# Kernel tuning notes

Measured on AMD Instinct MI355X. Metric: run time of the kernel, lower is better.

The kernel has to match this reference:

```python
import jax, jax.numpy as jnp
import numpy as np

B, NQ, NP = 4, 8192, 2048
DIM_INP, DIM, HID, OUT, NBLK = 256, 200, 128, 3, 5
VAR = 0.2 ** 2


def setup_inputs() -> dict:
    key = jax.random.key(0)
    ks = jax.random.split(key, 12)
    s = 0.05  # weight scale to keep activations sane
    return {
        "xyz_q": jax.random.uniform(ks[0], (B, NQ, 3), jnp.float32),
        "anchors": jax.random.uniform(ks[1], (B, NP, 3), jnp.float32),
        "anchor_feats": jax.random.normal(ks[2], (B, NP, DIM_INP), jnp.float32),
        "fc0_w": jax.random.normal(ks[3], (DIM_INP, DIM), jnp.float32) * s,
        "fc0_b": jnp.zeros((DIM,), jnp.float32),
        "fc1_w": jax.random.normal(ks[4], (DIM, HID), jnp.float32) * s,
        "fc1_b": jnp.zeros((HID,), jnp.float32),
        "blk_w0": jax.random.normal(ks[5], (NBLK, HID, HID), jnp.float32) * s,
        "blk_b0": jnp.zeros((NBLK, HID), jnp.float32),
        "blk_w1": jax.random.normal(ks[6], (NBLK, HID, HID), jnp.float32) * s,
        "blk_b1": jnp.zeros((NBLK, HID), jnp.float32),
        "fcc_w": jax.random.normal(ks[7], (NBLK, DIM, HID), jnp.float32) * s,
        "fcc_b": jnp.zeros((NBLK, HID), jnp.float32),
        "out_w": jax.random.normal(ks[8], (HID, OUT), jnp.float32) * s,
        "out_b": jnp.zeros((OUT,), jnp.float32),
    }


def reference(xyz_q, anchors, anchor_feats, fc0_w, fc0_b, fc1_w, fc1_b,
              blk_w0, blk_b0, blk_w1, blk_b1, fcc_w, fcc_b, out_w, out_b):
    relu = jax.nn.relu
    # Gaussian-kernel interpolation of anchor features at query points.
    # diff: [B, nq, np, 3]
    diff = anchors[:, None, :, :] - xyz_q[:, :, None, :]
    d = jnp.linalg.norm(diff, axis=-1)                    # [B, nq, np]
    logits = -((d + 1e-5) ** 2) / VAR
    weight = jax.nn.softmax(logits, axis=2)               # exp / sum, stable
    c = jnp.einsum('bqp,bpd->bqd', weight, anchor_feats)  # [B, nq, dim_inp]
    lat = c @ fc0_w + fc0_b                               # [B, nq, dim]
    net = relu(lat) @ fc1_w + fc1_b                       # [B, nq, hid]
    for i in range(NBLK):
        net = net + lat @ fcc_w[i] + fcc_b[i]
        # ResnetBlockFC: x + fc_1(relu(fc_0(relu(x))))
        dx = relu(relu(net) @ blk_w0[i] + blk_b0[i]) @ blk_w1[i] + blk_b1[i]
        net = net + dx
    return relu(net) @ out_w + out_b                      # [B, nq, 3]
```

## Files before the change

### kernel.cpp

```cpp
#include <hip/hip_runtime.h>
#include <math.h>

#define NP     2048
#define NQTOT  8192
#define DIN    256
#define DIM    200
#define HID    128
#define NOUT3  3
#define NBLK   5
#define TQ     32
#define NTHR   256
#define INVVAR 25.0f
#define NKT    (NP / 32)
#define NDT    (DIN / 16)
#define WSCALE 32768.0f
#define NFRAG  760

using f16x8 = __attribute__((ext_vector_type(8))) _Float16;
using f32x4 = __attribute__((ext_vector_type(4))) float;

__device__ __forceinline__ unsigned int pkrtz_u32(float a, float b) {
  auto p = __builtin_amdgcn_cvt_pkrtz(a, b);
  return __builtin_bit_cast(unsigned int, p);
}
__device__ __forceinline__ void pack_f16_2(const float* f, f16x8& h, f16x8& l) {
#pragma unroll
  for (int j = 0; j < 8; ++j) {
    const float v = f[j];
    const _Float16 hh = (_Float16)v;
    h[j] = hh; l[j] = (_Float16)(v - (float)hh);
  }
}
__device__ __forceinline__ void pack_w16(const float* f, f16x8& h, f16x8& l) {
#pragma unroll
  for (int j = 0; j < 8; ++j) {
    const float v = f[j] * WSCALE;
    const _Float16 hh = (_Float16)v;
    h[j] = hh; l[j] = (_Float16)(v - (float)hh);
  }
}
__device__ __forceinline__ void pack_a(const float* f, f16x8& h, f16x8& l) {
  union { f16x8 v; unsigned int u[4]; } H, L;
#pragma unroll
  for (int jp = 0; jp < 4; ++jp) {
    const float a = f[2 * jp], b = f[2 * jp + 1];
    auto hp = __builtin_amdgcn_cvt_pkrtz(a, b);
    H.u[jp] = __builtin_bit_cast(unsigned int, hp);
    L.u[jp] = pkrtz_u32(a - (float)hp[0], b - (float)hp[1]);
  }
  h = H.v; l = L.v;
}
__device__ __forceinline__ unsigned int split_pack(float x) {
  auto hp = __builtin_amdgcn_cvt_pkrtz(x, x);
  return pkrtz_u32(x, x - (float)hp[0]);
}

__device__ __forceinline__ int qsw(int r, int q) {
  return r * TQ + (q ^ (((r >> 2) & 7) << 2));
}
template<int KPAD>
__device__ __forceinline__ int sidx(int q, int k) {
  return q * KPAD + (((k >> 2) ^ (q & 7)) << 2) + (k & 3);
}

template<int KPAD, bool RELU>
__device__ __forceinline__ void store_split4(unsigned int* dst, int k, int qbase, f32x4 v) {
#pragma unroll
  for (int r = 0; r < 4; ++r) {
    float x = v[r];
    if (RELU) x = fmaxf(x, 0.f);
    dst[sidx<KPAD>(qbase + r, k)] = split_pack(x);
  }
}

__global__ __launch_bounds__(NTHR) void pid_packf(const float* __restrict__ F,
                                                  f16x8* __restrict__ wsHi,
                                                  f16x8* __restrict__ wsLo) {
  const int wid = threadIdx.x >> 6, l = threadIdx.x & 63;
  const int tile = blockIdx.x * 4 + wid;
  const int b  = tile >> 10;
  const int kt = (tile >> 4) & 63;
  const int dt = tile & 15;
  const int grp = l >> 4, qn = l & 15;
  const float* src = F + ((size_t)b * NP + kt * 32 + grp * 8) * DIN + dt * 16 + qn;
  float v[8];
#pragma unroll
  for (int j = 0; j < 8; ++j) v[j] = src[(size_t)j * DIN];
  f16x8 h, lo;
  pack_f16_2(v, h, lo);
  const size_t fi = (size_t)tile * 64 + l;
  wsHi[fi] = h; wsLo[fi] = lo;
}

__global__ __launch_bounds__(NTHR) void pid_packw(
    const float* __restrict__ fc0_w, const float* __restrict__ fc1_w,
    const float* __restrict__ fcc_w, const float* __restrict__ blk_w0,
    const float* __restrict__ blk_w1,
    f16x8* __restrict__ Wh, f16x8* __restrict__ Wm) {
  const int wid = threadIdx.x >> 6, l = threadIdx.x & 63;
  const int f = blockIdx.x * 4 + wid;
  if (f >= NFRAG) return;
  const float* src; int Kl, Nl, ks, nt;
  if (f < 104)      { int r = f;       src = fc0_w; Kl = 256; Nl = 200; ks = r / 13; nt = r % 13; }
  else if (f < 160) { int r = f - 104; src = fc1_w; Kl = 200; Nl = 128; ks = r / 8;  nt = r % 8; }
  else if (f < 440) { int r = f - 160; int i = r / 56; r %= 56;
                      src = fcc_w + (size_t)i * DIM * HID; Kl = 200; Nl = 128; ks = r / 8; nt = r % 8; }
  else if (f < 600) { int r = f - 440; int i = r / 32; r %= 32;
                      src = blk_w0 + (size_t)i * HID * HID; Kl = 128; Nl = 128; ks = r / 8; nt = r % 8; }
  else              { int r = f - 600; int i = r / 32; r %= 32;
                      src = blk_w1 + (size_t)i * HID * HID; Kl = 128; Nl = 128; ks = r / 8; nt = r % 8; }
  const int grp = l >> 4, n = nt * 16 + (l & 15);
  f16x8 h, m;
#pragma unroll
  for (int j = 0; j < 8; ++j) {
    const int k = ks * 32 + grp * 8 + j;
    const float v = (k < Kl && n < Nl) ? src[(size_t)k * Nl + n] : 0.f;
    const _Float16 hh = (_Float16)v;
    h[j] = hh; m[j] = (_Float16)(v - (float)hh);
  }
  const size_t fi = (size_t)f * 64 + l;
  Wh[fi] = h; Wm[fi] = m;
}

template<int KS, int NT, int MAXNT, int KPADIN, bool RELUA>
__device__ __forceinline__ void mm_stage(
    const unsigned int* __restrict__ Xs,
    const f16x8* __restrict__ Wh, const f16x8* __restrict__ Wm, int fbase,
    f32x4 acc[2][MAXNT], int wid, int l) {
  const int grp = l >> 4, qn = l & 15;
  f16x8 bhA[MAXNT], bmA[MAXNT], bhB[MAXNT], bmB[MAXNT];

#define LOADF(BH, BM, KSV)                                                    \
  _Pragma("unroll") for (int i = 0; i < MAXNT; ++i) {                         \
    const int nt = wid + i * 4;                                               \
    if (nt < NT) {                                                            \
      const size_t fi = (size_t)(fbase + (KSV) * NT + nt) * 64 + l;           \
      BH[i] = Wh[fi]; BM[i] = Wm[fi];                                         \
    }                                                                         \
  }

#define COMPUTE(KSV, BH, BM)                                                  \
  {                                                                           \
    const int u0 = (KSV) * 8 + grp * 2;                                       \
    f16x8 ah[2], al[2];                                                       \
    _Pragma("unroll") for (int qt = 0; qt < 2; ++qt) {                        \
      const int q = qt * 16 + qn;                                             \
      const unsigned int* row = Xs + q * KPADIN;                              \
      const uint4 lo = *(const uint4*)(row + (((u0) ^ (q & 7)) << 2));        \
      const uint4 hi = *(const uint4*)(row + (((u0 + 1) ^ (q & 7)) << 2));    \
      unsigned int p[8] = {lo.x, lo.y, lo.z, lo.w, hi.x, hi.y, hi.z, hi.w};   \
      if (RELUA) {                                                            \
        _Pragma("unroll") for (int j = 0; j < 8; ++j)                         \
          p[j] = (p[j] & 0x8000u) ? 0u : p[j];                                \
      }                                                                       \
      union { f16x8 v; unsigned int u[4]; } H, L;                             \
      _Pragma("unroll") for (int jp = 0; jp < 4; ++jp) {                      \
        H.u[jp] = __builtin_amdgcn_perm(p[2 * jp + 1], p[2 * jp], 0x05040100u);\
        L.u[jp] = __builtin_amdgcn_perm(p[2 * jp + 1], p[2 * jp], 0x07060302u);\
      }                                                                       \
      ah[qt] = H.v; al[qt] = L.v;                                             \
    }                                                                         \
    _Pragma("unroll") for (int qt = 0; qt < 2; ++qt)                          \
    _Pragma("unroll") for (int i = 0; i < MAXNT; ++i)                         \
      if (wid + i * 4 < NT) {                                                 \
        acc[qt][i] = __builtin_amdgcn_mfma_f32_16x16x32_f16(ah[qt], BH[i], acc[qt][i], 0, 0, 0); \
        acc[qt][i] = __builtin_amdgcn_mfma_f32_16x16x32_f16(ah[qt], BM[i], acc[qt][i], 0, 0, 0); \
        acc[qt][i] = __builtin_amdgcn_mfma_f32_16x16x32_f16(al[qt], BH[i], acc[qt][i], 0, 0, 0); \
      }                                                                       \
  }

  LOADF(bhA, bmA, 0)
#pragma unroll 1
  for (int ks = 0; ks + 1 < KS; ks += 2) {
    LOADF(bhB, bmB, ks + 1)
    COMPUTE(ks, bhA, bmA)
    if (ks + 2 < KS) { LOADF(bhA, bmA, ks + 2) }
    COMPUTE(ks + 1, bhB, bmB)
  }
  if (KS & 1) { COMPUTE(KS - 1, bhA, bmA) }
#undef LOADF
#undef COMPUTE
}

struct SMemV2 {
  union {
    struct { float ax[NP * 3]; float qx[TQ], qy[TQ], qz[TQ]; } a;
    unsigned int lats[32 * 224];
  } r1;
  union {
    unsigned int cTs[32 * 256];
    struct { unsigned int nets[32 * 128]; unsigned int tmps[32 * 128]; } nt;
    float netf[128 * 32];
  } r2;
  float sS[64];
};

__global__ __launch_bounds__(NTHR, 2) void pid_fused_mfma(
    const float* __restrict__ xyz_q, const float* __restrict__ anchors,
    const f16x8* __restrict__ wsFh, const f16x8* __restrict__ wsFl,
    const f16x8* __restrict__ Wh, const f16x8* __restrict__ Wm,
    const float* __restrict__ fc0_b, const float* __restrict__ fc1_b,
    const float* __restrict__ blk_b0, const float* __restrict__ blk_b1,
    const float* __restrict__ fcc_b,
    const float* __restrict__ out_w, const float* __restrict__ out_b,
    float* __restrict__ out) {
  __shared__ SMemV2 sm;
  const int t = threadIdx.x;
  const int bi = blockIdx.x;
  const int batch = bi & 3;
  const int q0 = (bi >> 2) * TQ;

  {
    const float4* src = (const float4*)(anchors + (size_t)batch * NP * 3);
    float4* dst = (float4*)sm.r1.a.ax;
#pragma unroll
    for (int j = 0; j < (NP * 3 / 4) / NTHR; ++j)
      dst[j * NTHR + t] = src[j * NTHR + t];
  }
  if (t < TQ) {
    const float* qp = xyz_q + ((size_t)batch * NQTOT + q0 + t) * 3;
    sm.r1.a.qx[t] = qp[0]; sm.r1.a.qy[t] = qp[1]; sm.r1.a.qz[t] = qp[2];
  }
  __syncthreads();

  const int wid = t >> 6, l = t & 63;
  const int kp = wid & 1;
  const int dh = wid >> 1;
  const int grp = l >> 4, qn = l & 15;
  const float q0x = sm.r1.a.qx[qn],      q0y = sm.r1.a.qy[qn],      q0z = sm.r1.a.qz[qn];
  const float q1x = sm.r1.a.qx[16 + qn], q1y = sm.r1.a.qy[16 + qn], q1z = sm.r1.a.qz[16 + qn];
  const float nC1 = -36.067376f;
  const float nC2 = -7.2134752e-4f;

  const size_t fb = (size_t)batch * (NKT * NDT * 64) + kp * 1024 + dh * 512 + l;
  const f16x8* pH0 = wsFh + fb;  const f16x8* pL0 = wsFl + fb;
  const f16x8* pH1 = pH0 + 256;  const f16x8* pL1 = pL0 + 256;

  f32x4 acc[2][8];
#pragma unroll
  for (int a = 0; a < 2; ++a)
#pragma unroll
    for (int j = 0; j < 8; ++j) acc[a][j] = (f32x4){0.f, 0.f, 0.f, 0.f};
  float s0 = 0.f, s1 = 0.f;

#pragma unroll 1
  for (int kt = kp; kt < NKT; kt += 2) {
    f16x8 bh0[4], bl0[4], bh1[4], bl1[4];
#pragma unroll
    for (int k = 0; k < 4; ++k) { bh0[k] = pH0[k * 64]; bl0[k] = pL0[k * 64]; }
#pragma unroll
    for (int k = 0; k < 4; ++k) { bh1[k] = pH1[k * 64]; bl1[k] = pL1[k * 64]; }

    const int pb = kt * 32 + grp * 8;
    float4 av[6];
    {
      const float4* ap = (const float4*)&sm.r1.a.ax[pb * 3];
#pragma unroll
      for (int j = 0; j < 6; ++j) av[j] = ap[j];
    }
    const float* af = (const float*)av;
    float w8[8];
#pragma unroll
    for (int j = 0; j < 8; ++j) {
      const float dx = af[3 * j] - q0x, dy = af[3 * j + 1] - q0y, dz = af[3 * j + 2] - q0z;
      const float D = fmaf(dx, dx, fmaf(dy, dy, dz * dz));
      const float s = __builtin_amdgcn_sqrtf(D);
      const float u = __builtin_amdgcn_exp2f(fmaf(nC2, s, fmaf(nC1, D, 15.0f)));
      w8[j] = u; s0 += u;
    }
    f16x8 ah0, al0;
    pack_a(w8, ah0, al0);
#pragma unroll
    for (int j = 0; j < 8; ++j) {
      const float dx = af[3 * j] - q1x, dy = af[3 * j + 1] - q1y, dz = af[3 * j + 2] - q1z;
      const float D = fmaf(dx, dx, fmaf(dy, dy, dz * dz));
      const float s = __builtin_amdgcn_sqrtf(D);
      const float u = __builtin_amdgcn_exp2f(fmaf(nC2, s, fmaf(nC1, D, 15.0f)));
      w8[j] = u; s1 += u;
    }
    f16x8 ah1, al1;
    pack_a(w8, ah1, al1);

#define MM3(ACC, AH, AL, BH, BL)                                              \
    ACC = __builtin_amdgcn_mfma_f32_16x16x32_f16(AH, BH, ACC, 0, 0, 0);       \
    ACC = __builtin_amdgcn_mfma_f32_16x16x32_f16(AH, BL, ACC, 0, 0, 0);       \
    ACC = __builtin_amdgcn_mfma_f32_16x16x32_f16(AL, BH, ACC, 0, 0, 0);
#pragma unroll
    for (int k = 0; k < 4; ++k) {
      MM3(acc[0][k], ah0, al0, bh0[k], bl0[k])
      MM3(acc[1][k], ah1, al1, bh0[k], bl0[k])
    }
#pragma unroll
    for (int k = 0; k < 4; ++k) {
      MM3(acc[0][4 + k], ah0, al0, bh1[k], bl1[k])
      MM3(acc[1][4 + k], ah1, al1, bh1[k], bl1[k])
    }
#undef MM3
    pH0 += 2048; pL0 += 2048; pH1 += 2048; pL1 += 2048;
  }

  s0 += __shfl_xor(s0, 16); s0 += __shfl_xor(s0, 32);
  s1 += __shfl_xor(s1, 16); s1 += __shfl_xor(s1, 32);
  if (dh == 0 && l < 16) {
    sm.sS[kp * 32 + qn] = s0;
    sm.sS[kp * 32 + 16 + qn] = s1;
  }
  float4* P = (float4*)sm.r2.cTs;
  if (kp == 0) {
#pragma unroll
    for (int qt2 = 0; qt2 < 2; ++qt2)
#pragma unroll
      for (int d2 = 0; d2 < 8; ++d2)
        P[(qt2 * 16 + dh * 8 + d2) * 64 + grp * 16 + qn] =
            make_float4(acc[qt2][d2][0], acc[qt2][d2][1],
                        acc[qt2][d2][2], acc[qt2][d2][3]);
  }
  __syncthreads();
  if (kp == 1) {
#pragma unroll
    for (int qt2 = 0; qt2 < 2; ++qt2)
#pragma unroll
      for (int d2 = 0; d2 < 8; ++d2) {
        const float4 pv = P[(qt2 * 16 + dh * 8 + d2) * 64 + grp * 16 + qn];
        acc[qt2][d2][0] += pv.x; acc[qt2][d2][1] += pv.y;
        acc[qt2][d2][2] += pv.z; acc[qt2][d2][3] += pv.w;
      }
  } else {
    const int lid = (wid >> 1) * 64 + l;
#pragma unroll
    for (int z = 0; z < 6; ++z) {
      const int idx = lid * 6 + z;
      const int q = idx / 24, kk = 200 + idx % 24;
      sm.r1.lats[sidx<224>(q, kk)] = 0u;
    }
  }
  __syncthreads();
  if (kp == 1) {
    float sc0[4], sc1[4];
#pragma unroll
    for (int r = 0; r < 4; ++r) {
      const int j = grp * 4 + r;
      sc0[r] = __builtin_amdgcn_rcpf(sm.sS[j] + sm.sS[32 + j]);
      sc1[r] = __builtin_amdgcn_rcpf(sm.sS[16 + j] + sm.sS[48 + j]);
    }
#pragma unroll
    for (int d2 = 0; d2 < 8; ++d2) {
      const int k = (dh * 8 + d2) * 16 + qn;
      const f32x4 v0 = {acc[0][d2][0] * sc0[0], acc[0][d2][1] * sc0[1],
                        acc[0][d2][2] * sc0[2], acc[0][d2][3] * sc0[3]};
      store_split4<256, false>(sm.r2.cTs, k, grp * 4, v0);
      const f32x4 v1 = {acc[1][d2][0] * sc1[0], acc[1][d2][1] * sc1[1],
                        acc[1][d2][2] * sc1[2], acc[1][d2][3] * sc1[3]};
      store_split4<256, false>(sm.r2.cTs, k, 16 + grp * 4, v1);
    }
  }
  __syncthreads();

  {
    f32x4 a0[2][4];
#pragma unroll
    for (int i = 0; i < 4; ++i) {
      const int nt = wid + i * 4;
      if (nt < 13) {
        const int n = nt * 16 + qn;
        const float b = (n < 200) ? fc0_b[n] : 0.f;
#pragma unroll
        for (int q2 = 0; q2 < 2; ++q2) a0[q2][i] = (f32x4){b, b, b, b};
      }
    }
    mm_stage<8, 13, 4, 256, false>(sm.r2.cTs, Wh, Wm, 0, a0, wid, l);
#pragma unroll
    for (int q2 = 0; q2 < 2; ++q2)
#pragma unroll
      for (int i = 0; i < 4; ++i) {
        const int nt = wid + i * 4;
        if (nt < 13)
          store_split4<224, false>(sm.r1.lats, nt * 16 + qn, q2 * 16 + grp * 4, a0[q2][i]);
      }
  }
  __syncthreads();

  f32x4 net[2][2];
#pragma unroll
  for (int i = 0; i < 2; ++i) {
    const float b = fc1_b[(wid + i * 4) * 16 + qn];
#pragma unroll
    for (int q2 = 0; q2 < 2; ++q2) net[q2][i] = (f32x4){b, b, b, b};
  }
  mm_stage<7, 8, 2, 224, true>(sm.r1.lats, Wh, Wm, 104, net, wid, l);

#pragma unroll 1
  for (int ib = 0; ib < NBLK; ++ib) {
#pragma unroll
    for (int i = 0; i < 2; ++i) {
      const float b = fcc_b[ib * HID + (wid + i * 4) * 16 + qn];
#pragma unroll
      for (int q2 = 0; q2 < 2; ++q2) net[q2][i] += (f32x4){b, b, b, b};
    }
    mm_stage<7, 8, 2, 224, false>(sm.r1.lats, Wh, Wm, 160 + 56 * ib, net, wid, l);
#pragma unroll
    for (int q2 = 0; q2 < 2; ++q2)
#pragma unroll
      for (int i = 0; i < 2; ++i)
        store_split4<128, true>(sm.r2.nt.nets, (wid + i * 4) * 16 + qn,
                                q2 * 16 + grp * 4, net[q2][i]);
    __syncthreads();
    f32x4 a2[2][2];
#pragma unroll
    for (int i = 0; i < 2; ++i) {
      const float b = blk_b0[ib * HID + (wid + i * 4) * 16 + qn];
#pragma unroll
      for (int q2 = 0; q2 < 2; ++q2) a2[q2][i] = (f32x4){b, b, b, b};
    }
    mm_stage<4, 8, 2, 128, false>(sm.r2.nt.nets, Wh, Wm, 440 + 32 * ib, a2, wid, l);
#pragma unroll
    for (int q2 = 0; q2 < 2; ++q2)
#pragma unroll
      for (int i = 0; i < 2; ++i)
        store_split4<128, true>(sm.r2.nt.tmps, (wid + i * 4) * 16 + qn,
                                q2 * 16 + grp * 4, a2[q2][i]);
    __syncthreads();
#pragma unroll
    for (int i = 0; i < 2; ++i) {
      const float b = blk_b1[ib * HID + (wid + i * 4) * 16 + qn];
#pragma unroll
      for (int q2 = 0; q2 < 2; ++q2) net[q2][i] += (f32x4){b, b, b, b};
    }
    mm_stage<4, 8, 2, 128, false>(sm.r2.nt.tmps, Wh, Wm, 600 + 32 * ib, net, wid, l);
  }
  __syncthreads();

#pragma unroll
  for (int q2 = 0; q2 < 2; ++q2)
#pragma unroll
    for (int i = 0; i < 2; ++i) {
      const int n = (wid + i * 4) * 16 + qn;
      *(float4*)&sm.r2.netf[n * 32 + q2 * 16 + grp * 4] =
          make_float4(net[q2][i][0], net[q2][i][1], net[q2][i][2], net[q2][i][3]);
    }
  __syncthreads();
  if (t < TQ * NOUT3) {
    const int q = t / NOUT3, n = t - q * NOUT3;
    float s = out_b[n];
#pragma unroll 8
    for (int k = 0; k < HID; ++k)
      s = fmaf(fmaxf(sm.r2.netf[k * 32 + q], 0.f), out_w[k * NOUT3 + n], s);
    out[((size_t)batch * NQTOT + q0 + q) * NOUT3 + n] = s;
  }
}

template<int K, bool RELUX, bool ACCY>
__device__ __forceinline__ void stage_h128(const float* __restrict__ X,
                                           const float* __restrict__ Wg,
                                           const float* __restrict__ bg,
                                           float* __restrict__ Y, int t) {
  const int qg = t & 7, ng = t >> 3;
  const int n0 = ng * 4, q0 = qg * 4;
  const float4 bv = *(const float4*)&bg[n0];
  const float br[4] = {bv.x, bv.y, bv.z, bv.w};
  float acc[4][4];
#pragma unroll
  for (int j = 0; j < 4; ++j) {
    if (ACCY) {
      const float4 yv = *(const float4*)&Y[qsw(n0 + j, q0)];
      acc[0][j] = yv.x + br[j]; acc[1][j] = yv.y + br[j];
      acc[2][j] = yv.z + br[j]; acc[3][j] = yv.w + br[j];
    } else {
      acc[0][j] = br[j]; acc[1][j] = br[j]; acc[2][j] = br[j]; acc[3][j] = br[j];
    }
  }
#pragma unroll 2
  for (int k0 = 0; k0 < K; k0 += 8) {
    float4 wr[8];
#pragma unroll
    for (int kk = 0; kk < 8; ++kk)
      wr[kk] = *(const float4*)&Wg[(size_t)(k0 + kk) * HID + n0];
#pragma unroll
    for (int kk = 0; kk < 8; ++kk) {
      float4 xv = *(const float4*)&X[qsw(k0 + kk, q0)];
      if (RELUX) {
        xv.x = fmaxf(xv.x, 0.f); xv.y = fmaxf(xv.y, 0.f);
        xv.z = fmaxf(xv.z, 0.f); xv.w = fmaxf(xv.w, 0.f);
      }
      const float xr[4] = {xv.x, xv.y, xv.z, xv.w};
      const float wl[4] = {wr[kk].x, wr[kk].y, wr[kk].z, wr[kk].w};
#pragma unroll
      for (int i = 0; i < 4; ++i)
#pragma unroll
        for (int j = 0; j < 4; ++j)
          acc[i][j] = fmaf(xr[i], wl[j], acc[i][j]);
    }
  }
#pragma unroll
  for (int j = 0; j < 4; ++j)
    *(float4*)&Y[qsw(n0 + j, q0)] =
        make_float4(acc[0][j], acc[1][j], acc[2][j], acc[3][j]);
}

__device__ __forceinline__ void stage_fc0v(const float* __restrict__ X,
                                           const float* __restrict__ Wg,
                                           const float* __restrict__ bg,
                                           float* __restrict__ Y, int t) {
  const int qg = t & 7, ng = t >> 3;
  const int n0 = ng * 8, q0 = qg * 4;
  const bool act = (ng < 25);
  float acc[4][8];
  if (act) {
    const float4 b0 = *(const float4*)&bg[n0];
    const float4 b1 = *(const float4*)&bg[n0 + 4];
    const float br[8] = {b0.x, b0.y, b0.z, b0.w, b1.x, b1.y, b1.z, b1.w};
#pragma unroll
    for (int j = 0; j < 8; ++j)
#pragma unroll
      for (int i = 0; i < 4; ++i) acc[i][j] = br[j];
  }
#pragma unroll 2
  for (int k0 = 0; k0 < DIN; k0 += 4) {
    if (act) {
      float4 wa[4], wb[4];
#pragma unroll
      for (int kk = 0; kk < 4; ++kk) {
        wa[kk] = *(const float4*)&Wg[(size_t)(k0 + kk) * DIM + n0];
        wb[kk] = *(const float4*)&Wg[(size_t)(k0 + kk) * DIM + n0 + 4];
      }
#pragma unroll
      for (int kk = 0; kk < 4; ++kk) {
        const float4 xv = *(const float4*)&X[qsw(k0 + kk, q0)];
        const float xr[4] = {xv.x, xv.y, xv.z, xv.w};
        const float wl[8] = {wa[kk].x, wa[kk].y, wa[kk].z, wa[kk].w,
                             wb[kk].x, wb[kk].y, wb[kk].z, wb[kk].w};
#pragma unroll
        for (int i = 0; i < 4; ++i)
#pragma unroll
          for (int j = 0; j < 8; ++j)
            acc[i][j] = fmaf(xr[i], wl[j], acc[i][j]);
      }
    }
  }
  if (act) {
#pragma unroll
    for (int j = 0; j < 8; ++j)
      *(float4*)&Y[qsw(n0 + j, q0)] =
          make_float4(acc[0][j], acc[1][j], acc[2][j], acc[3][j]);
  }
}

struct SA1 {
  float ax[NP * 3];
  float qx[TQ], qy[TQ], qz[TQ], m[TQ];
  float sred[8 * TQ];
};
struct SB1 {
  float lat[DIM * TQ];
  union {
    float cT[DIN * TQ];
    struct { float net[HID * TQ]; float tmp[HID * TQ]; } nt;
  } u;
};
struct SMem1 { union { SA1 a; SB1 b; } s; float sS[TQ]; };

__global__ __launch_bounds__(NTHR, 2) void pid_fused_vec(
    const float* __restrict__ xyz_q, const float* __restrict__ anchors,
    const f16x8* __restrict__ wsFh, const f16x8* __restrict__ wsFl,
    const float* __restrict__ fc0_w, const float* __restrict__ fc0_b,
    const float* __restrict__ fc1_w, const float* __restrict__ fc1_b,
    const float* __restrict__ blk_w0, const float* __restrict__ blk_b0,
    const float* __restrict__ blk_w1, const float* __restrict__ blk_b1,
    const float* __restrict__ fcc_w, const float* __restrict__ fcc_b,
    const float* __restrict__ out_w, const float* __restrict__ out_b,
    float* __restrict__ out) {
  __shared__ SMem1 sm;
  const int t = threadIdx.x;
  const int bi = blockIdx.x;
  const int batch = bi & 3;
  const int q0 = (bi >> 2) * TQ;

  {
    const float4* src = (const float4*)(anchors + (size_t)batch * NP * 3);
    float4* dst = (float4*)sm.s.a.ax;
#pragma unroll
    for (int j = 0; j < (NP * 3 / 4) / NTHR; ++j)
      dst[j * NTHR + t] = src[j * NTHR + t];
  }
  if (t < TQ) {
    const float* qp = xyz_q + ((size_t)batch * NQTOT + q0 + t) * 3;
    sm.s.a.qx[t] = qp[0]; sm.s.a.qy[t] = qp[1]; sm.s.a.qz[t] = qp[2];
  }
  __syncthreads();
  {
    const int q = t & 31, g = t >> 5;
    const float qxv = sm.s.a.qx[q], qyv = sm.s.a.qy[q], qzv = sm.s.a.qz[q];
    float mloc = 3.0e38f;
    const float* az = sm.s.a.ax + g * 256 * 3;
    for (int pi = 0; pi < 256; ++pi) {
      const float dx = az[pi * 3 + 0] - qxv;
      const float dy = az[pi * 3 + 1] - qyv;
      const float dz = az[pi * 3 + 2] - qzv;
      mloc = fminf(mloc, fmaf(dx, dx, fmaf(dy, dy, dz * dz)));
    }
    sm.s.a.sred[g * TQ + q] = mloc;
  }
  __syncthreads();
  if (t < TQ) {
    float mv = sm.s.a.sred[t];
#pragma unroll
    for (int g = 1; g < 8; ++g) mv = fminf(mv, sm.s.a.sred[g * TQ + t]);
    const float dmin = sqrtf(mv) + 1e-5f;
    sm.s.a.m[t] = -dmin * dmin * INVVAR;
  }
  __syncthreads();

  const int wid = t >> 6, l = t & 63;
  const int qt = wid & 1;
  const int dgb = (wid >> 1) * 8;
  const int grp = l >> 4, qn = l & 15;
  const float qxv = sm.s.a.qx[qt * 16 + qn];
  const float qyv = sm.s.a.qy[qt * 16 + qn];
  const float qzv = sm.s.a.qz[qt * 16 + qn];
  const float negm = -sm.s.a.m[qt * 16 + qn];
  const f16x8* BH = wsFh + (size_t)batch * NKT * NDT * 64;
  const f16x8* BL = wsFl + (size_t)batch * NKT * NDT * 64;

  f32x4 acc[8];
#pragma unroll
  for (int j = 0; j < 8; ++j) acc[j] = (f32x4){0.f, 0.f, 0.f, 0.f};
  float ssum = 0.f;
#pragma unroll 1
  for (int kt = 0; kt < NKT; ++kt) {
    f16x8 bh[8], bl[8];
#pragma unroll
    for (int d2 = 0; d2 < 8; ++d2) {
      const size_t fi = ((size_t)kt * NDT + dgb + d2) * 64 + l;
      bh[d2] = BH[fi]; bl[d2] = BL[fi];
    }
    const int pb = kt * 32 + grp * 8;
    float4 av[6];
    {
      const float4* ap = (const float4*)&sm.s.a.ax[pb * 3];
#pragma unroll
      for (int j = 0; j < 6; ++j) av[j] = ap[j];
    }
    const float* af = (const float*)av;
    float w8[8];
#pragma unroll
    for (int j = 0; j < 8; ++j) {
      const float dx = af[3 * j] - qxv, dy = af[3 * j + 1] - qyv, dz = af[3 * j + 2] - qzv;
      const float d = sqrtf(fmaf(dx, dx, fmaf(dy, dy, dz * dz))) + 1e-5f;
      const float u = __expf(fmaf(d * d, -INVVAR, negm));
      w8[j] = u; ssum += u;
    }
    f16x8 ah, al;
    pack_w16(w8, ah, al);
#pragma unroll
    for (int d2 = 0; d2 < 8; ++d2)
      acc[d2] = __builtin_amdgcn_mfma_f32_16x16x32_f16(ah, bh[d2], acc[d2], 0, 0, 0);
#pragma unroll
    for (int d2 = 0; d2 < 8; ++d2)
      acc[d2] = __builtin_amdgcn_mfma_f32_16x16x32_f16(ah, bl[d2], acc[d2], 0, 0, 0);
#pragma unroll
    for (int d2 = 0; d2 < 8; ++d2)
      acc[d2] = __builtin_amdgcn_mfma_f32_16x16x32_f16(al, bh[d2], acc[d2], 0, 0, 0);
  }
  ssum += __shfl_xor(ssum, 16);
  ssum += __shfl_xor(ssum, 32);
  if (wid < 2 && grp == 0) sm.sS[qt * 16 + qn] = ssum;
  __syncthreads();
  float sc[4];
#pragma unroll
  for (int r = 0; r < 4; ++r)
    sc[r] = (1.0f / WSCALE) / sm.sS[qt * 16 + grp * 4 + r];
#pragma unroll
  for (int d2 = 0; d2 < 8; ++d2) {
    const int d = (dgb + d2) * 16 + qn;
    *(float4*)&sm.s.b.u.cT[qsw(d, qt * 16 + grp * 4)] =
        make_float4(acc[d2][0] * sc[0], acc[d2][1] * sc[1],
                    acc[d2][2] * sc[2], acc[d2][3] * sc[3]);
  }
  __syncthreads();

  stage_fc0v(sm.s.b.u.cT, fc0_w, fc0_b, sm.s.b.lat, t);
  __syncthreads();
  stage_h128<DIM, true, false>(sm.s.b.lat, fc1_w, fc1_b, sm.s.b.u.nt.net, t);
  __syncthreads();
#pragma unroll 1
  for (int i = 0; i < NBLK; ++i) {
    stage_h128<DIM, false, true>(sm.s.b.lat, fcc_w + (size_t)i * DIM * HID,
                                 fcc_b + i * HID, sm.s.b.u.nt.net, t);
    __syncthreads();
    stage_h128<HID, true, false>(sm.s.b.u.nt.net, blk_w0 + (size_t)i * HID * HID,
                                 blk_b0 + i * HID, sm.s.b.u.nt.tmp, t);
    __syncthreads();
    stage_h128<HID, true, true>(sm.s.b.u.nt.tmp, blk_w1 + (size_t)i * HID * HID,
                                blk_b1 + i * HID, sm.s.b.u.nt.net, t);
    __syncthreads();
  }
  if (t < TQ * NOUT3) {
    const int q = t / NOUT3, n = t - q * NOUT3;
    float s = out_b[n];
    const float* net = sm.s.b.u.nt.net;
#pragma unroll 8
    for (int k = 0; k < HID; ++k)
      s = fmaf(fmaxf(net[k * TQ + (q ^ (((k >> 2) & 7) << 2))], 0.f),
               out_w[k * NOUT3 + n], s);
    out[((size_t)batch * NQTOT + q0 + q) * NOUT3 + n] = s;
  }
}

extern "C" void kernel_launch(void* const* d_in, const int* in_sizes, int n_in,
                              void* d_out, int out_size, void* d_ws, size_t ws_size,
                              hipStream_t stream) {
  (void)in_sizes; (void)n_in; (void)out_size;
  const float* xyz_q        = (const float*)d_in[0];
  const float* anchors      = (const float*)d_in[1];
  const float* anchor_feats = (const float*)d_in[2];
  const float* fc0_w        = (const float*)d_in[3];
  const float* fc0_b        = (const float*)d_in[4];
  const float* fc1_w        = (const float*)d_in[5];
  const float* fc1_b        = (const float*)d_in[6];
  const float* blk_w0       = (const float*)d_in[7];
  const float* blk_b0       = (const float*)d_in[8];
  const float* blk_w1       = (const float*)d_in[9];
  const float* blk_b1       = (const float*)d_in[10];
  const float* fcc_w        = (const float*)d_in[11];
  const float* fcc_b        = (const float*)d_in[12];
  const float* out_w        = (const float*)d_in[13];
  const float* out_b        = (const float*)d_in[14];
  float* out = (float*)d_out;

  const size_t F_BYTES = (size_t)4 * NKT * NDT * 64 * 16;
  const size_t W_BYTES = (size_t)NFRAG * 64 * 16;
  f16x8* wsFh = (f16x8*)d_ws;
  f16x8* wsFl = (f16x8*)((char*)d_ws + F_BYTES);
  f16x8* Wh   = (f16x8*)((char*)d_ws + 2 * F_BYTES);
  f16x8* Wm   = (f16x8*)((char*)d_ws + 2 * F_BYTES + W_BYTES);

  hipLaunchKernelGGL(pid_packf, dim3(1024), dim3(NTHR), 0, stream,
                     anchor_feats, wsFh, wsFl);
  if (ws_size >= 2 * F_BYTES + 2 * W_BYTES) {
    hipLaunchKernelGGL(pid_packw, dim3((NFRAG + 3) / 4), dim3(NTHR), 0, stream,
                       fc0_w, fc1_w, fcc_w, blk_w0, blk_w1, Wh, Wm);
    hipLaunchKernelGGL(pid_fused_mfma, dim3(1024), dim3(NTHR), 0, stream,
                       xyz_q, anchors, wsFh, wsFl, Wh, Wm,
                       fc0_b, fc1_b, blk_b0, blk_b1, fcc_b, out_w, out_b, out);
  } else {
    hipLaunchKernelGGL(pid_fused_vec, dim3(1024), dim3(NTHR), 0, stream,
                       xyz_q, anchors, wsFh, wsFl,
                       fc0_w, fc0_b, fc1_w, fc1_b, blk_w0, blk_b0,
                       blk_w1, blk_b1, fcc_w, fcc_b, out_w, out_b, out);
  }
}
```

Baseline: 252.6 us.

## Double-buffer weight and activation loads and raise MFMA priority

The interpolation loop now double-buffers the per-tile B-fragment global loads, so the next tile's weights are fetched while the current tile's Gaussian weights are computed and multiplied. The MLP stage helper also prefetches its LDS activation rows alongside the weight fragments one k-step ahead. MFMA sections are wrapped in s_setprio so waves issuing matrix ops get scheduling priority. This hides global and LDS latency at the cost of extra VGPRs, which may hurt occupancy or cause spills under the 2-waves launch bound.

```diff
diff --git a/kernel.cpp b/kernel.cpp
--- a/kernel.cpp
+++ b/kernel.cpp
@@ -128,9 +128,13 @@
     const f16x8* __restrict__ Wh, const f16x8* __restrict__ Wm, int fbase,
     f32x4 acc[2][MAXNT], int wid, int l) {
   const int grp = l >> 4, qn = l & 15;
+  const int xr = qn & 7;
+  const unsigned int* row0 = Xs + qn * KPADIN;
+  const unsigned int* row1 = Xs + (16 + qn) * KPADIN;
   f16x8 bhA[MAXNT], bmA[MAXNT], bhB[MAXNT], bmB[MAXNT];
-
-#define LOADF(BH, BM, KSV)                                                    \
+  uint4 aLoA[2], aHiA[2], aLoB[2], aHiB[2];
+
+#define LOADW(BH, BM, KSV)                                                    \
   _Pragma("unroll") for (int i = 0; i < MAXNT; ++i) {                         \
     const int nt = wid + i * 4;                                               \
     if (nt < NT) {                                                            \
@@ -139,16 +143,21 @@
     }                                                                         \
   }
 
-#define COMPUTE(KSV, BH, BM)                                                  \
+#define LOADA(ALO, AHI, KSV)                                                  \
   {                                                                           \
     const int u0 = (KSV) * 8 + grp * 2;                                       \
+    ALO[0] = *(const uint4*)(row0 + ((u0 ^ xr) << 2));                        \
+    AHI[0] = *(const uint4*)(row0 + (((u0 + 1) ^ xr) << 2));                  \
+    ALO[1] = *(const uint4*)(row1 + ((u0 ^ xr) << 2));                        \
+    AHI[1] = *(const uint4*)(row1 + (((u0 + 1) ^ xr) << 2));                  \
+  }
+
+#define COMPUTE(BH, BM, ALO, AHI)                                             \
+  {                                                                           \
     f16x8 ah[2], al[2];                                                       \
     _Pragma("unroll") for (int qt = 0; qt < 2; ++qt) {                        \
-      const int q = qt * 16 + qn;                                             \
-      const unsigned int* row = Xs + q * KPADIN;                              \
-      const uint4 lo = *(const uint4*)(row + (((u0) ^ (q & 7)) << 2));        \
-      const uint4 hi = *(const uint4*)(row + (((u0 + 1) ^ (q & 7)) << 2));    \
-      unsigned int p[8] = {lo.x, lo.y, lo.z, lo.w, hi.x, hi.y, hi.z, hi.w};   \
+      unsigned int p[8] = {ALO[qt].x, ALO[qt].y, ALO[qt].z, ALO[qt].w,        \
+                           AHI[qt].x, AHI[qt].y, AHI[qt].z, AHI[qt].w};       \
       if (RELUA) {                                                            \
         _Pragma("unroll") for (int j = 0; j < 8; ++j)                         \
           p[j] = (p[j] & 0x8000u) ? 0u : p[j];                                \
@@ -160,6 +169,7 @@
       }                                                                       \
       ah[qt] = H.v; al[qt] = L.v;                                             \
     }                                                                         \
+    __builtin_amdgcn_s_setprio(1);                                            \
     _Pragma("unroll") for (int qt = 0; qt < 2; ++qt)                          \
     _Pragma("unroll") for (int i = 0; i < MAXNT; ++i)                         \
       if (wid + i * 4 < NT) {                                                 \
@@ -167,18 +177,20 @@
         acc[qt][i] = __builtin_amdgcn_mfma_f32_16x16x32_f16(ah[qt], BM[i], acc[qt][i], 0, 0, 0); \
         acc[qt][i] = __builtin_amdgcn_mfma_f32_16x16x32_f16(al[qt], BH[i], acc[qt][i], 0, 0, 0); \
       }                                                                       \
-  }
-
-  LOADF(bhA, bmA, 0)
+    __builtin_amdgcn_s_setprio(0);                                            \
+  }
+
+  LOADW(bhA, bmA, 0) LOADA(aLoA, aHiA, 0)
 #pragma unroll 1
   for (int ks = 0; ks + 1 < KS; ks += 2) {
-    LOADF(bhB, bmB, ks + 1)
-    COMPUTE(ks, bhA, bmA)
-    if (ks + 2 < KS) { LOADF(bhA, bmA, ks + 2) }
-    COMPUTE(ks + 1, bhB, bmB)
-  }
-  if (KS & 1) { COMPUTE(KS - 1, bhA, bmA) }
-#undef LOADF
+    LOADW(bhB, bmB, ks + 1) LOADA(aLoB, aHiB, ks + 1)
+    COMPUTE(bhA, bmA, aLoA, aHiA)
+    if (ks + 2 < KS) { LOADW(bhA, bmA, ks + 2) LOADA(aLoA, aHiA, ks + 2) }
+    COMPUTE(bhB, bmB, aLoB, aHiB)
+  }
+  if (KS & 1) { COMPUTE(bhA, bmA, aLoA, aHiA) }
+#undef LOADW
+#undef LOADA
 #undef COMPUTE
 }
 
@@ -243,61 +255,77 @@
     for (int j = 0; j < 8; ++j) acc[a][j] = (f32x4){0.f, 0.f, 0.f, 0.f};
   float s0 = 0.f, s1 = 0.f;
 
-#pragma unroll 1
-  for (int kt = kp; kt < NKT; kt += 2) {
-    f16x8 bh0[4], bl0[4], bh1[4], bl1[4];
-#pragma unroll
-    for (int k = 0; k < 4; ++k) { bh0[k] = pH0[k * 64]; bl0[k] = pL0[k * 64]; }
-#pragma unroll
-    for (int k = 0; k < 4; ++k) { bh1[k] = pH1[k * 64]; bl1[k] = pL1[k * 64]; }
-
-    const int pb = kt * 32 + grp * 8;
-    float4 av[6];
-    {
-      const float4* ap = (const float4*)&sm.r1.a.ax[pb * 3];
-#pragma unroll
-      for (int j = 0; j < 6; ++j) av[j] = ap[j];
-    }
-    const float* af = (const float*)av;
-    float w8[8];
-#pragma unroll
-    for (int j = 0; j < 8; ++j) {
-      const float dx = af[3 * j] - q0x, dy = af[3 * j + 1] - q0y, dz = af[3 * j + 2] - q0z;
-      const float D = fmaf(dx, dx, fmaf(dy, dy, dz * dz));
-      const float s = __builtin_amdgcn_sqrtf(D);
-      const float u = __builtin_amdgcn_exp2f(fmaf(nC2, s, fmaf(nC1, D, 15.0f)));
-      w8[j] = u; s0 += u;
-    }
-    f16x8 ah0, al0;
-    pack_a(w8, ah0, al0);
-#pragma unroll
-    for (int j = 0; j < 8; ++j) {
-      const float dx = af[3 * j] - q1x, dy = af[3 * j + 1] - q1y, dz = af[3 * j + 2] - q1z;
-      const float D = fmaf(dx, dx, fmaf(dy, dy, dz * dz));
-      const float s = __builtin_amdgcn_sqrtf(D);
-      const float u = __builtin_amdgcn_exp2f(fmaf(nC2, s, fmaf(nC1, D, 15.0f)));
-      w8[j] = u; s1 += u;
-    }
-    f16x8 ah1, al1;
-    pack_a(w8, ah1, al1);
+  f16x8 Xh0[4], Xl0[4], Xh1[4], Xl1[4];
+  f16x8 Yh0[4], Yl0[4], Yh1[4], Yl1[4];
+
+#define LOADB(H0, L0, H1, L1)                                                 \
+  {                                                                           \
+    _Pragma("unroll") for (int k = 0; k < 4; ++k) {                           \
+      H0[k] = pH0[k * 64]; L0[k] = pL0[k * 64];                               \
+      H1[k] = pH1[k * 64]; L1[k] = pL1[k * 64];                               \
+    }                                                                         \
+    pH0 += 2048; pL0 += 2048; pH1 += 2048; pL1 += 2048;                       \
+  }
 
 #define MM3(ACC, AH, AL, BH, BL)                                              \
     ACC = __builtin_amdgcn_mfma_f32_16x16x32_f16(AH, BH, ACC, 0, 0, 0);       \
     ACC = __builtin_amdgcn_mfma_f32_16x16x32_f16(AH, BL, ACC, 0, 0, 0);       \
     ACC = __builtin_amdgcn_mfma_f32_16x16x32_f16(AL, BH, ACC, 0, 0, 0);
-#pragma unroll
-    for (int k = 0; k < 4; ++k) {
-      MM3(acc[0][k], ah0, al0, bh0[k], bl0[k])
-      MM3(acc[1][k], ah1, al1, bh0[k], bl0[k])
-    }
-#pragma unroll
-    for (int k = 0; k < 4; ++k) {
-      MM3(acc[0][4 + k], ah0, al0, bh1[k], bl1[k])
-      MM3(acc[1][4 + k], ah1, al1, bh1[k], bl1[k])
-    }
+
+#define ASTEP(TI, H0, L0, H1, L1)                                             \
+  {                                                                           \
+    const int pb = (kp + 2 * (TI)) * 32 + grp * 8;                            \
+    float4 av[6];                                                             \
+    {                                                                         \
+      const float4* ap = (const float4*)&sm.r1.a.ax[pb * 3];                  \
+      _Pragma("unroll") for (int j = 0; j < 6; ++j) av[j] = ap[j];            \
+    }                                                                         \
+    const float* af = (const float*)av;                                       \
+    float w8[8];                                                              \
+    _Pragma("unroll") for (int j = 0; j < 8; ++j) {                           \
+      const float dx = af[3 * j] - q0x, dy = af[3 * j + 1] - q0y,             \
+                  dz = af[3 * j + 2] - q0z;                                   \
+      const float D = fmaf(dx, dx, fmaf(dy, dy, dz * dz));                    \
+      const float s = __builtin_amdgcn_sqrtf(D);                              \
+      const float u = __builtin_amdgcn_exp2f(fmaf(nC2, s, fmaf(nC1, D, 15.0f)));\
+      w8[j] = u; s0 += u;                                                     \
+    }                                                                         \
+    f16x8 ah0, al0; pack_a(w8, ah0, al0);                                     \
+    _Pragma("unroll") for (int j = 0; j < 8; ++j) {                           \
+      const float dx = af[3 * j] - q1x, dy = af[3 * j + 1] - q1y,             \
+                  dz = af[3 * j + 2] - q1z;                                   \
+      const float D = fmaf(dx, dx, fmaf(dy, dy, dz * dz));                    \
+      const float s = __builtin_amdgcn_sqrtf(D);                              \
+      const float u = __builtin_amdgcn_exp2f(fmaf(nC2, s, fmaf(nC1, D, 15.0f)));\
+      w8[j] = u; s1 += u;                                                     \
+    }                                                                         \
+    f16x8 ah1, al1; pack_a(w8, ah1, al1);                                     \
+    __builtin_amdgcn_s_setprio(1);                                            \
+    _Pragma("unroll") for (int k = 0; k < 4; ++k) {                           \
+      MM3(acc[0][k], ah0, al0, H0[k], L0[k])                                  \
+      MM3(acc[1][k], ah1, al1, H0[k], L0[k])                                  \
+    }                                                                         \
+    _Pragma("unroll") for (int k = 0; k < 4; ++k) {                           \
+      MM3(acc[0][4 + k], ah0, al0, H1[k], L1[k])                              \
+      MM3(acc[1][4 + k], ah1, al1, H1[k], L1[k])                              \
+    }                                                                         \
+    __builtin_amdgcn_s_setprio(0);                                            \
+  }
+
+  LOADB(Xh0, Xl0, Xh1, Xl1)
+#pragma unroll 1
+  for (int ti = 0; ti + 2 < 32; ti += 2) {
+    LOADB(Yh0, Yl0, Yh1, Yl1)
+    ASTEP(ti, Xh0, Xl0, Xh1, Xl1)
+    LOADB(Xh0, Xl0, Xh1, Xl1)
+    ASTEP(ti + 1, Yh0, Yl0, Yh1, Yl1)
+  }
+  LOADB(Yh0, Yl0, Yh1, Yl1)
+  ASTEP(30, Xh0, Xl0, Xh1, Xl1)
+  ASTEP(31, Yh0, Yl0, Yh1, Yl1)
+#undef ASTEP
 #undef MM3
-    pH0 += 2048; pL0 += 2048; pH1 += 2048; pL1 += 2048;
-  }
+#undef LOADB
 
   s0 += __shfl_xor(s0, 16); s0 += __shfl_xor(s0, 32);
   s1 += __shfl_xor(s1, 16); s1 += __shfl_xor(s1, 32);
```

New measurement: 624.4 us. +147.2%, slower.

## Fold fc0 weight into anchor features before softmax interpolation

Applied to the files above, without the earlier changes.

Uses linearity of the weighted sum to precompute anchor_feats @ fc0_w per batch in a new pre-pass kernel, so the interpolation produces the 200-wide latent directly instead of the 256-wide feature. This shrinks the interpolation MFMA work from 16 to 14 column tiles and removes the whole fc0 matmul stage, along with its weights and one barrier. The bias is added after normalisation. The cost is an extra fp32 SIMT GEMM over 8192 anchor rows in the pre-pass, plus the rounding of the precomputed product to split fp16.

```diff
diff --git a/kernel.cpp b/kernel.cpp
--- a/kernel.cpp
+++ b/kernel.cpp
@@ -12,9 +12,11 @@
 #define NTHR   256
 #define INVVAR 25.0f
 #define NKT    (NP / 32)
-#define NDT    (DIN / 16)
+#define NDT    16
+#define NDT2   14
+#define LATK   224
 #define WSCALE 32768.0f
-#define NFRAG  760
+#define NFRAG  656
 
 using f16x8 = __attribute__((ext_vector_type(8))) _Float16;
 using f32x4 = __attribute__((ext_vector_type(4))) float;
@@ -62,7 +64,6 @@
 __device__ __forceinline__ int sidx(int q, int k) {
   return q * KPAD + (((k >> 2) ^ (q & 7)) << 2) + (k & 3);
 }
-
 template<int KPAD, bool RELU>
 __device__ __forceinline__ void store_split4(unsigned int* dst, int k, int qbase, f32x4 v) {
 #pragma unroll
@@ -73,9 +74,69 @@
   }
 }
 
-__global__ __launch_bounds__(NTHR) void pid_packf(const float* __restrict__ F,
-                                                  f16x8* __restrict__ wsHi,
-                                                  f16x8* __restrict__ wsLo) {
+struct PFW { float Fc[32][32]; float Wc[32][LATK]; };
+__global__ __launch_bounds__(NTHR) void pid_packfw(
+    const float* __restrict__ F, const float* __restrict__ W0,
+    _Float16* __restrict__ wsHi, _Float16* __restrict__ wsLo) {
+  __shared__ PFW s;
+  const int t = threadIdx.x;
+  const int batch = blockIdx.x >> 6, kt = blockIdx.x & 63;
+  const int p = t >> 3, ng = t & 7;
+  const int n0 = ng * 28;
+  float acc[28];
+#pragma unroll
+  for (int j = 0; j < 28; ++j) acc[j] = 0.f;
+
+#pragma unroll 1
+  for (int kc = 0; kc < 8; ++kc) {
+    __syncthreads();
+    {
+      const int pp = t >> 3, k4 = t & 7;
+      *(float4*)&s.Fc[pp][k4 * 4] =
+          *(const float4*)&F[((size_t)batch * NP + kt * 32 + pp) * DIN + kc * 32 + k4 * 4];
+    }
+    {
+#pragma unroll
+      for (int c = 0; c < 7; ++c) {
+        const int idx = c * 256 + t;
+        const int kk = idx / 56, c4 = idx % 56;
+        const int n4 = c4 * 4;
+        float4 v = make_float4(0.f, 0.f, 0.f, 0.f);
+        if (n4 < DIM)
+          v = *(const float4*)&W0[(size_t)(kc * 32 + kk) * DIM + n4];
+        *(float4*)&s.Wc[kk][n4] = v;
+      }
+    }
+    __syncthreads();
+#pragma unroll 4
+    for (int k = 0; k < 32; ++k) {
+      const float fv = s.Fc[p][k];
+#pragma unroll
+      for (int c = 0; c < 7; ++c) {
+        const float4 w = *(const float4*)&s.Wc[k][n0 + 4 * c];
+        acc[4 * c + 0] = fmaf(fv, w.x, acc[4 * c + 0]);
+        acc[4 * c + 1] = fmaf(fv, w.y, acc[4 * c + 1]);
+        acc[4 * c + 2] = fmaf(fv, w.z, acc[4 * c + 2]);
+        acc[4 * c + 3] = fmaf(fv, w.w, acc[4 * c + 3]);
+      }
+    }
+  }
+  const int grp = p >> 3, jj = p & 7;
+#pragma unroll
+  for (int j2 = 0; j2 < 28; ++j2) {
+    const int n = n0 + j2, dt = n >> 4, qn = n & 15;
+    const size_t base =
+        (((size_t)(batch * 64 + kt) * NDT2 + dt) * 64 + grp * 16 + qn) * 8 + jj;
+    const float v = acc[j2];
+    const _Float16 hh = (_Float16)v;
+    wsHi[base] = hh;
+    wsLo[base] = (_Float16)(v - (float)hh);
+  }
+}
+
+__global__ __launch_bounds__(NTHR) void pid_packf16(const float* __restrict__ F,
+                                                    f16x8* __restrict__ wsHi,
+                                                    f16x8* __restrict__ wsLo) {
   const int wid = threadIdx.x >> 6, l = threadIdx.x & 63;
   const int tile = blockIdx.x * 4 + wid;
   const int b  = tile >> 10;
@@ -93,21 +154,19 @@
 }
 
 __global__ __launch_bounds__(NTHR) void pid_packw(
-    const float* __restrict__ fc0_w, const float* __restrict__ fc1_w,
-    const float* __restrict__ fcc_w, const float* __restrict__ blk_w0,
-    const float* __restrict__ blk_w1,
+    const float* __restrict__ fc1_w, const float* __restrict__ fcc_w,
+    const float* __restrict__ blk_w0, const float* __restrict__ blk_w1,
     f16x8* __restrict__ Wh, f16x8* __restrict__ Wm) {
   const int wid = threadIdx.x >> 6, l = threadIdx.x & 63;
   const int f = blockIdx.x * 4 + wid;
   if (f >= NFRAG) return;
   const float* src; int Kl, Nl, ks, nt;
-  if (f < 104)      { int r = f;       src = fc0_w; Kl = 256; Nl = 200; ks = r / 13; nt = r % 13; }
-  else if (f < 160) { int r = f - 104; src = fc1_w; Kl = 200; Nl = 128; ks = r / 8;  nt = r % 8; }
-  else if (f < 440) { int r = f - 160; int i = r / 56; r %= 56;
+  if (f < 56)       { int r = f;       src = fc1_w; Kl = 200; Nl = 128; ks = r / 8; nt = r % 8; }
+  else if (f < 336) { int r = f - 56;  int i = r / 56; r %= 56;
                       src = fcc_w + (size_t)i * DIM * HID; Kl = 200; Nl = 128; ks = r / 8; nt = r % 8; }
-  else if (f < 600) { int r = f - 440; int i = r / 32; r %= 32;
+  else if (f < 496) { int r = f - 336; int i = r / 32; r %= 32;
                       src = blk_w0 + (size_t)i * HID * HID; Kl = 128; Nl = 128; ks = r / 8; nt = r % 8; }
-  else              { int r = f - 600; int i = r / 32; r %= 32;
+  else              { int r = f - 496; int i = r / 32; r %= 32;
                       src = blk_w1 + (size_t)i * HID * HID; Kl = 128; Nl = 128; ks = r / 8; nt = r % 8; }
   const int grp = l >> 4, n = nt * 16 + (l & 15);
   f16x8 h, m;
@@ -185,10 +244,10 @@
 struct SMemV2 {
   union {
     struct { float ax[NP * 3]; float qx[TQ], qy[TQ], qz[TQ]; } a;
-    unsigned int lats[32 * 224];
+    unsigned int lats[32 * LATK];
   } r1;
   union {
-    unsigned int cTs[32 * 256];
+    float4 exch[28 * 64];
     struct { unsigned int nets[32 * 128]; unsigned int tmps[32 * 128]; } nt;
     float netf[128 * 32];
   } r2;
@@ -232,24 +291,21 @@
   const float nC1 = -36.067376f;
   const float nC2 = -7.2134752e-4f;
 
-  const size_t fb = (size_t)batch * (NKT * NDT * 64) + kp * 1024 + dh * 512 + l;
-  const f16x8* pH0 = wsFh + fb;  const f16x8* pL0 = wsFl + fb;
-  const f16x8* pH1 = pH0 + 256;  const f16x8* pL1 = pL0 + 256;
-
-  f32x4 acc[2][8];
+  const f16x8* pH = wsFh + ((size_t)(batch * 64 + kp) * NDT2 + dh * 7) * 64 + l;
+  const f16x8* pL = wsFl + ((size_t)(batch * 64 + kp) * NDT2 + dh * 7) * 64 + l;
+
+  f32x4 acc[2][7];
 #pragma unroll
   for (int a = 0; a < 2; ++a)
 #pragma unroll
-    for (int j = 0; j < 8; ++j) acc[a][j] = (f32x4){0.f, 0.f, 0.f, 0.f};
+    for (int j = 0; j < 7; ++j) acc[a][j] = (f32x4){0.f, 0.f, 0.f, 0.f};
   float s0 = 0.f, s1 = 0.f;
 
 #pragma unroll 1
   for (int kt = kp; kt < NKT; kt += 2) {
-    f16x8 bh0[4], bl0[4], bh1[4], bl1[4];
-#pragma unroll
-    for (int k = 0; k < 4; ++k) { bh0[k] = pH0[k * 64]; bl0[k] = pL0[k * 64]; }
-#pragma unroll
-    for (int k = 0; k < 4; ++k) { bh1[k] = pH1[k * 64]; bl1[k] = pL1[k * 64]; }
+    f16x8 bh[7], bl[7];
+#pragma unroll
+    for (int k = 0; k < 7; ++k) { bh[k] = pH[k * 64]; bl[k] = pL[k * 64]; }
 
     const int pb = kt * 32 + grp * 8;
     float4 av[6];
@@ -286,17 +342,12 @@
     ACC = __builtin_amdgcn_mfma_f32_16x16x32_f16(AH, BL, ACC, 0, 0, 0);       \
     ACC = __builtin_amdgcn_mfma_f32_16x16x32_f16(AL, BH, ACC, 0, 0, 0);
 #pragma unroll
-    for (int k = 0; k < 4; ++k) {
-      MM3(acc[0][k], ah0, al0, bh0[k], bl0[k])
-      MM3(acc[1][k], ah1, al1, bh0[k], bl0[k])
-    }
-#pragma unroll
-    for (int k = 0; k < 4; ++k) {
-      MM3(acc[0][4 + k], ah0, al0, bh1[k], bl1[k])
-      MM3(acc[1][4 + k], ah1, al1, bh1[k], bl1[k])
+    for (int k = 0; k < 7; ++k) {
+      MM3(acc[0][k], ah0, al0, bh[k], bl[k])
+      MM3(acc[1][k], ah1, al1, bh[k], bl[k])
     }
 #undef MM3
-    pH0 += 2048; pL0 += 2048; pH1 += 2048; pL1 += 2048;
+    pH += 2 * NDT2 * 64; pL += 2 * NDT2 * 64;
   }
 
   s0 += __shfl_xor(s0, 16); s0 += __shfl_xor(s0, 32);
@@ -305,34 +356,15 @@
     sm.sS[kp * 32 + qn] = s0;
     sm.sS[kp * 32 + 16 + qn] = s1;
   }
-  float4* P = (float4*)sm.r2.cTs;
+  float4* P = sm.r2.exch;
   if (kp == 0) {
 #pragma unroll
     for (int qt2 = 0; qt2 < 2; ++qt2)
 #pragma unroll
-      for (int d2 = 0; d2 < 8; ++d2)
-        P[(qt2 * 16 + dh * 8 + d2) * 64 + grp * 16 + qn] =
+      for (int d2 = 0; d2 < 7; ++d2)
+        P[(qt2 * 14 + dh * 7 + d2) * 64 + grp * 16 + qn] =
             make_float4(acc[qt2][d2][0], acc[qt2][d2][1],
                         acc[qt2][d2][2], acc[qt2][d2][3]);
-  }
-  __syncthreads();
-  if (kp == 1) {
-#pragma unroll
-    for (int qt2 = 0; qt2 < 2; ++qt2)
-#pragma unroll
-      for (int d2 = 0; d2 < 8; ++d2) {
-        const float4 pv = P[(qt2 * 16 + dh * 8 + d2) * 64 + grp * 16 + qn];
-        acc[qt2][d2][0] += pv.x; acc[qt2][d2][1] += pv.y;
-        acc[qt2][d2][2] += pv.z; acc[qt2][d2][3] += pv.w;
-      }
-  } else {
-    const int lid = (wid >> 1) * 64 + l;
-#pragma unroll
-    for (int z = 0; z < 6; ++z) {
-      const int idx = lid * 6 + z;
-      const int q = idx / 24, kk = 200 + idx % 24;
-      sm.r1.lats[sidx<224>(q, kk)] = 0u;
-    }
   }
   __syncthreads();
   if (kp == 1) {
@@ -344,39 +376,22 @@
       sc1[r] = __builtin_amdgcn_rcpf(sm.sS[16 + j] + sm.sS[48 + j]);
     }
 #pragma unroll
-    for (int d2 = 0; d2 < 8; ++d2) {
-      const int k = (dh * 8 + d2) * 16 + qn;
-      const f32x4 v0 = {acc[0][d2][0] * sc0[0], acc[0][d2][1] * sc0[1],
-                        acc[0][d2][2] * sc0[2], acc[0][d2][3] * sc0[3]};
-      store_split4<256, false>(sm.r2.cTs, k, grp * 4, v0);
-      const f32x4 v1 = {acc[1][d2][0] * sc1[0], acc[1][d2][1] * sc1[1],
-                        acc[1][d2][2] * sc1[2], acc[1][d2][3] * sc1[3]};
-      store_split4<256, false>(sm.r2.cTs, k, 16 + grp * 4, v1);
-    }
-  }
-  __syncthreads();
-
-  {
-    f32x4 a0[2][4];
-#pragma unroll
-    for (int i = 0; i < 4; ++i) {
-      const int nt = wid + i * 4;
-      if (nt < 13) {
-        const int n = nt * 16 + qn;
-        const float b = (n < 200) ? fc0_b[n] : 0.f;
-#pragma unroll
-        for (int q2 = 0; q2 < 2; ++q2) a0[q2][i] = (f32x4){b, b, b, b};
-      }
-    }
-    mm_stage<8, 13, 4, 256, false>(sm.r2.cTs, Wh, Wm, 0, a0, wid, l);
-#pragma unroll
-    for (int q2 = 0; q2 < 2; ++q2)
-#pragma unroll
-      for (int i = 0; i < 4; ++i) {
-        const int nt = wid + i * 4;
-        if (nt < 13)
-          store_split4<224, false>(sm.r1.lats, nt * 16 + qn, q2 * 16 + grp * 4, a0[q2][i]);
-      }
+    for (int d2 = 0; d2 < 7; ++d2) {
+      const int k = (dh * 7 + d2) * 16 + qn;
+      const float bb = (k < DIM) ? fc0_b[k] : 0.f;
+      const float4 p0 = P[(0 * 14 + dh * 7 + d2) * 64 + grp * 16 + qn];
+      const float4 p1 = P[(1 * 14 + dh * 7 + d2) * 64 + grp * 16 + qn];
+      const f32x4 v0 = {fmaf(acc[0][d2][0] + p0.x, sc0[0], bb),
+                        fmaf(acc[0][d2][1] + p0.y, sc0[1], bb),
+                        fmaf(acc[0][d2][2] + p0.z, sc0[2], bb),
+                        fmaf(acc[0][d2][3] + p0.w, sc0[3], bb)};
+      store_split4<LATK, false>(sm.r1.lats, k, grp * 4, v0);
+      const f32x4 v1 = {fmaf(acc[1][d2][0] + p1.x, sc1[0], bb),
+                        fmaf(acc[1][d2][1] + p1.y, sc1[1], bb),
+                        fmaf(acc[1][d2][2] + p1.z, sc1[2], bb),
+                        fmaf(acc[1][d2][3] + p1.w, sc1[3], bb)};
+      store_split4<LATK, false>(sm.r1.lats, k, 16 + grp * 4, v1);
+    }
   }
   __syncthreads();
 
@@ -387,7 +402,7 @@
 #pragma unroll
     for (int q2 = 0; q2 < 2; ++q2) net[q2][i] = (f32x4){b, b, b, b};
   }
-  mm_stage<7, 8, 2, 224, true>(sm.r1.lats, Wh, Wm, 104, net, wid, l);
+  mm_stage<7, 8, 2, LATK, true>(sm.r1.lats, Wh, Wm, 0, net, wid, l);
 
 #pragma unroll 1
   for (int ib = 0; ib < NBLK; ++ib) {
@@ -397,7 +412,7 @@
 #pragma unroll
       for (int q2 = 0; q2 < 2; ++q2) net[q2][i] += (f32x4){b, b, b, b};
     }
-    mm_stage<7, 8, 2, 224, false>(sm.r1.lats, Wh, Wm, 160 + 56 * ib, net, wid, l);
+    mm_stage<7, 8, 2, LATK, false>(sm.r1.lats, Wh, Wm, 56 + 56 * ib, net, wid, l);
 #pragma unroll
     for (int q2 = 0; q2 < 2; ++q2)
 #pragma unroll
@@ -412,7 +427,7 @@
 #pragma unroll
       for (int q2 = 0; q2 < 2; ++q2) a2[q2][i] = (f32x4){b, b, b, b};
     }
-    mm_stage<4, 8, 2, 128, false>(sm.r2.nt.nets, Wh, Wm, 440 + 32 * ib, a2, wid, l);
+    mm_stage<4, 8, 2, 128, false>(sm.r2.nt.nets, Wh, Wm, 336 + 32 * ib, a2, wid, l);
 #pragma unroll
     for (int q2 = 0; q2 < 2; ++q2)
 #pragma unroll
@@ -426,7 +441,7 @@
 #pragma unroll
       for (int q2 = 0; q2 < 2; ++q2) net[q2][i] += (f32x4){b, b, b, b};
     }
-    mm_stage<4, 8, 2, 128, false>(sm.r2.nt.tmps, Wh, Wm, 600 + 32 * ib, net, wid, l);
+    mm_stage<4, 8, 2, 128, false>(sm.r2.nt.tmps, Wh, Wm, 496 + 32 * ib, net, wid, l);
   }
   __syncthreads();
 
@@ -727,22 +742,26 @@
   const float* out_b        = (const float*)d_in[14];
   float* out = (float*)d_out;
 
-  const size_t F_BYTES = (size_t)4 * NKT * NDT * 64 * 16;
-  const size_t W_BYTES = (size_t)NFRAG * 64 * 16;
-  f16x8* wsFh = (f16x8*)d_ws;
-  f16x8* wsFl = (f16x8*)((char*)d_ws + F_BYTES);
-  f16x8* Wh   = (f16x8*)((char*)d_ws + 2 * F_BYTES);
-  f16x8* Wm   = (f16x8*)((char*)d_ws + 2 * F_BYTES + W_BYTES);
-
-  hipLaunchKernelGGL(pid_packf, dim3(1024), dim3(NTHR), 0, stream,
-                     anchor_feats, wsFh, wsFl);
-  if (ws_size >= 2 * F_BYTES + 2 * W_BYTES) {
+  const size_t F2_BYTES = (size_t)4 * 64 * NDT2 * 64 * 16;
+  const size_t W2_BYTES = (size_t)NFRAG * 64 * 16;
+  if (ws_size >= 2 * F2_BYTES + 2 * W2_BYTES) {
+    f16x8* wsFh = (f16x8*)d_ws;
+    f16x8* wsFl = (f16x8*)((char*)d_ws + F2_BYTES);
+    f16x8* Wh   = (f16x8*)((char*)d_ws + 2 * F2_BYTES);
+    f16x8* Wm   = (f16x8*)((char*)d_ws + 2 * F2_BYTES + W2_BYTES);
+    hipLaunchKernelGGL(pid_packfw, dim3(256), dim3(NTHR), 0, stream,
+                       anchor_feats, fc0_w, (_Float16*)wsFh, (_Float16*)wsFl);
     hipLaunchKernelGGL(pid_packw, dim3((NFRAG + 3) / 4), dim3(NTHR), 0, stream,
-                       fc0_w, fc1_w, fcc_w, blk_w0, blk_w1, Wh, Wm);
+                       fc1_w, fcc_w, blk_w0, blk_w1, Wh, Wm);
     hipLaunchKernelGGL(pid_fused_mfma, dim3(1024), dim3(NTHR), 0, stream,
                        xyz_q, anchors, wsFh, wsFl, Wh, Wm,
                        fc0_b, fc1_b, blk_b0, blk_b1, fcc_b, out_w, out_b, out);
   } else {
+    const size_t F1_BYTES = (size_t)4 * NKT * NDT * 64 * 16;
+    f16x8* wsFh = (f16x8*)d_ws;
+    f16x8* wsFl = (f16x8*)((char*)d_ws + F1_BYTES);
+    hipLaunchKernelGGL(pid_packf16, dim3(1024), dim3(NTHR), 0, stream,
+                       anchor_feats, wsFh, wsFl);
     hipLaunchKernelGGL(pid_fused_vec, dim3(1024), dim3(NTHR), 0, stream,
                        xyz_q, anchors, wsFh, wsFl,
                        fc0_w, fc0_b, fc1_w, fc1_b, blk_w0, blk_b0,
```

Result: slower. 340.2 us (+34.7%).
